# Performance work log

Measured on AMD Instinct MI355X. Metric: run time of the kernel, lower is better.

## Reference

```python
import jax, jax.numpy as jnp
import numpy as np

TOP_K = 2
EPS = 1e-9


def setup_inputs() -> dict:
    key = jax.random.key(0)
    k1, k2, k3, k4 = jax.random.split(key, 4)
    B, T, D, H, E = 4, 2048, 1024, 4096, 8
    x = jax.random.normal(k1, (B, T, D), dtype=jnp.float32)
    Wr = jax.random.normal(k2, (D, E), dtype=jnp.float32) * 0.02
    W1 = jax.random.normal(k3, (E, D, H), dtype=jnp.float32) * 0.02
    W2 = jax.random.normal(k4, (E, H, D), dtype=jnp.float32) * 0.02
    return {"x": x, "Wr": Wr, "W1": W1, "W2": W2}


def reference(x, Wr, W1, W2):
    # x: (B,T,D); Wr: (D,E); W1: (E,D,H); W2: (E,H,D)
    E = Wr.shape[1]
    logits = jnp.einsum('btd,de->bte', x, Wr)          # (B,T,E)
    probs = jax.nn.softmax(logits, axis=-1)
    top_p, top_i = jax.lax.top_k(probs, TOP_K)         # (B,T,K)
    gates = top_p / (jnp.sum(top_p, axis=-1, keepdims=True) + EPS)
    # combine weights per expert: (B,T,E), zero where expert not selected
    oh = jax.nn.one_hot(top_i, E, dtype=x.dtype)       # (B,T,K,E)
    comb = jnp.sum(oh * gates[..., None], axis=2)      # (B,T,E)
    out = jnp.zeros_like(x)
    for e in range(E):  # fixed small expert loop
        h = jax.nn.gelu(jnp.einsum('btd,dh->bth', x, W1[e]), approximate=False)
        y = jnp.einsum('bth,hd->btd', h, W2[e])
        out = out + comb[..., e:e + 1] * y
    # load-balancing loss (on detached stats, matching torch .detach())
    mask = (jnp.sum(oh, axis=2) > 0).astype(jnp.float32)  # (B,T,E)
    imp = jnp.sum(jax.lax.stop_gradient(probs), axis=(0, 1))
    load = jnp.sum(jax.lax.stop_gradient(mask), axis=(0, 1))
    imp = imp / (jnp.sum(imp) + EPS)
    load = load / (jnp.sum(load) + EPS)
    lb = jnp.sum(imp * load) * E
    return out, lb
```

## Files before the change

### kernel.cpp

```cpp
#include <hip/hip_runtime.h>
#include <hip/hip_bf16.h>
#include <math.h>

#define NTOK 8192
#define DDIM 1024
#define HDIM 4096
#define NEXP 8
#define HROWS (NTOK*2 + 256)
#define RBLK 512

typedef unsigned int u32;
typedef unsigned short u16;
typedef __bf16 bf16x8 __attribute__((ext_vector_type(8)));
typedef float f32x4 __attribute__((ext_vector_type(4)));
typedef u32 u32x4 __attribute__((ext_vector_type(4)));
typedef u16 u16x8 __attribute__((ext_vector_type(8)));
typedef u16 u16x4 __attribute__((ext_vector_type(4)));

__device__ __forceinline__ u16 f2bf(float f){
  u32 u = __builtin_bit_cast(u32, f);
  u32 r = (u + 0x7FFFu + ((u >> 16) & 1u)) >> 16;
  return (u16)r;
}
__device__ __forceinline__ float bf2f(u16 b){
  u32 u = ((u32)b) << 16;
  return __builtin_bit_cast(float, u);
}
__device__ __forceinline__ void gl_lds16(const void* g, void* l){
  __builtin_amdgcn_global_load_lds(
      (const __attribute__((address_space(1))) u32*)g,
      (__attribute__((address_space(3))) u32*)l, 16, 0, 0);
}
__device__ __forceinline__ float gelu_t(float v){
  float u = v * (0.7978845608f + 0.0356774081f * v * v);
  float e = __expf(2.0f * u);
  float t = 1.0f - 2.0f / (e + 1.0f);
  return 0.5f * v * (1.0f + t);
}

__global__ __launch_bounds__(256) void transpose_cvt(const float* __restrict__ in,
                                                     u16* __restrict__ out,
                                                     int R, int C){
  int e = blockIdx.z;
  const float* pin = in + (long)e * R * C;
  u16* pout = out + (long)e * R * C;
  __shared__ u16 tile[64][65];
  int c0 = blockIdx.x * 64, r0 = blockIdx.y * 64;
  int tid = threadIdx.x;
#pragma unroll
  for (int j = 0; j < 4; j++){
    int idx = tid + 256 * j;
    int r = idx >> 4, c4 = (idx & 15) << 2;
    float4 v = *(const float4*)(pin + (long)(r0 + r) * C + c0 + c4);
    tile[r][c4]     = f2bf(v.x);
    tile[r][c4 + 1] = f2bf(v.y);
    tile[r][c4 + 2] = f2bf(v.z);
    tile[r][c4 + 3] = f2bf(v.w);
  }
  __syncthreads();
#pragma unroll
  for (int j = 0; j < 4; j++){
    int idx = tid + 256 * j;
    int orow = idx >> 4, c4 = (idx & 15) << 2;
    u16x4 o;
    o[0] = tile[c4][orow];     o[1] = tile[c4 + 1][orow];
    o[2] = tile[c4 + 2][orow]; o[3] = tile[c4 + 3][orow];
    *(u16x4*)(pout + (long)(c0 + orow) * R + r0 + c4) = o;
  }
}

__global__ __launch_bounds__(1024) void route_kernel(const float* __restrict__ x,
                                                     const float* __restrict__ Wr,
                                                     u16* __restrict__ xb,
                                                     int4* __restrict__ meta,
                                                     float2* __restrict__ gates,
                                                     int* __restrict__ selrk,
                                                     int* __restrict__ blockhist,
                                                     float* __restrict__ impPart){
  const int wid = threadIdx.x >> 6;
  const int lane = threadIdx.x & 63;
  const int t = blockIdx.x * 16 + wid;
  const float* xr = x + (long)t * DDIM;
  u16* xbr = xb + (long)t * DDIM;
  float acc[NEXP] = {};
  for (int d0 = lane * 4; d0 < DDIM; d0 += 256){
    float4 xv = *(const float4*)(xr + d0);
    u16x4 xo;
    xo[0] = f2bf(xv.x); xo[1] = f2bf(xv.y); xo[2] = f2bf(xv.z); xo[3] = f2bf(xv.w);
    *(u16x4*)(xbr + d0) = xo;
    const float* w = Wr + d0 * NEXP;
#pragma unroll
    for (int q = 0; q < 4; q++){
      float xq = ((const float*)&xv)[q];
      float4 w0 = *(const float4*)(w + q * NEXP);
      float4 w1 = *(const float4*)(w + q * NEXP + 4);
      acc[0] += xq * w0.x; acc[1] += xq * w0.y; acc[2] += xq * w0.z; acc[3] += xq * w0.w;
      acc[4] += xq * w1.x; acc[5] += xq * w1.y; acc[6] += xq * w1.z; acc[7] += xq * w1.w;
    }
  }
#pragma unroll
  for (int e = 0; e < NEXP; e++){
#pragma unroll
    for (int off = 32; off; off >>= 1) acc[e] += __shfl_xor(acc[e], off, 64);
  }
  __shared__ int sel_s[32];
  __shared__ float p_s[16][NEXP];
  if (lane == 0){
    float mx = acc[0];
#pragma unroll
    for (int e = 1; e < NEXP; e++) mx = fmaxf(mx, acc[e]);
    float p[NEXP]; float s = 0.f;
#pragma unroll
    for (int e = 0; e < NEXP; e++){ p[e] = expf(acc[e] - mx); s += p[e]; }
    float inv = 1.f / s;
#pragma unroll
    for (int e = 0; e < NEXP; e++){ p[e] *= inv; p_s[wid][e] = p[e]; }
    int i0 = 0; float v0 = p[0];
#pragma unroll
    for (int e = 1; e < NEXP; e++) if (p[e] > v0){ v0 = p[e]; i0 = e; }
    int i1 = -1; float v1 = -1.f;
#pragma unroll
    for (int e = 0; e < NEXP; e++) if (e != i0 && p[e] > v1){ v1 = p[e]; i1 = e; }
    float gs = v0 + v1 + 1e-9f;
    meta[t] = make_int4(i0, i1, 0, 0);
    gates[t] = make_float2(v0 / gs, v1 / gs);
    sel_s[wid * 2] = i0;
    sel_s[wid * 2 + 1] = i1;
  }
  __syncthreads();
  const int tid = threadIdx.x;
  if (tid < 32){
    int e = sel_s[tid];
    int r = 0;
    for (int m = 0; m < tid; m++) r += (sel_s[m] == e) ? 1 : 0;
    selrk[blockIdx.x * 32 + tid] = (r << 3) | e;
  }
  if (tid < NEXP){
    int hcount = 0;
#pragma unroll
    for (int m = 0; m < 32; m++) hcount += (sel_s[m] == tid) ? 1 : 0;
    blockhist[blockIdx.x * NEXP + tid] = hcount;
    float s = 0.f;
#pragma unroll
    for (int w = 0; w < 16; w++) s += p_s[w][tid];
    impPart[blockIdx.x * NEXP + tid] = s;
  }
}

__global__ __launch_bounds__(512) void scan_kernel(int* __restrict__ blockhist,
                                                   const float* __restrict__ impPart,
                                                   int* __restrict__ cnt,
                                                   int* __restrict__ offs,
                                                   float* __restrict__ imp){
  const int e = threadIdx.x >> 6;
  const int lane = threadIdx.x & 63;
  const int base = lane * 8;
  int v[8]; int s = 0;
#pragma unroll
  for (int i = 0; i < 8; i++){
    int tmp = blockhist[(base + i) * NEXP + e];
    v[i] = s; s += tmp;
  }
  int inc = s;
#pragma unroll
  for (int off = 1; off < 64; off <<= 1){
    int o = __shfl_up(inc, off, 64);
    if (lane >= off) inc += o;
  }
  int excl = inc - s;
#pragma unroll
  for (int i = 0; i < 8; i++) blockhist[(base + i) * NEXP + e] = v[i] + excl;
  int tot = __shfl(inc, 63, 64);
  float fs = 0.f;
#pragma unroll
  for (int i = 0; i < 8; i++) fs += impPart[(base + i) * NEXP + e];
#pragma unroll
  for (int off = 32; off; off >>= 1) fs += __shfl_xor(fs, off, 64);
  __shared__ int cnt_s[NEXP];
  if (lane == 0){ cnt_s[e] = tot; cnt[e] = tot; imp[e] = fs; }
  __syncthreads();
  if (threadIdx.x == 0){
    int o = 0;
    for (int q = 0; q < NEXP; q++){ offs[q] = o; o += cnt_s[q]; }
  }
}

__global__ __launch_bounds__(256) void fill_kernel(const int* __restrict__ selrk,
                                                   const int* __restrict__ blockhist,
                                                   int* __restrict__ elist,
                                                   int4* __restrict__ meta){
  int m = blockIdx.x * 256 + threadIdx.x;
  int t = m >> 1, c = m & 1, b = m >> 5;
  int pk = selrk[m];
  int e = pk & 7, r = pk >> 3;
  int gslot = blockhist[b * NEXP + e] + r;
  elist[e * NTOK + gslot] = t;
  ((int*)meta)[t * 4 + 2 + c] = gslot;
}

template<int KD, int ND, int TG, bool GATHER, bool GELU>
__global__ __launch_bounds__(512, 4) void gemm_tb(const u16* __restrict__ Ag,
                                                  const u16* __restrict__ Bg,
                                                  u16* __restrict__ Cg,
                                                  const int* __restrict__ elist,
                                                  const int* __restrict__ cnt,
                                                  const int* __restrict__ offs){
  const int NDB = ND / 256;
  const int bid = blockIdx.x;
  const int e  = bid & 7;
  const int le = bid >> 3;
  const int tti = le % TG;
  const int db  = (le / TG) % NDB;
  const int tg  = le / (TG * NDB);
  const int tt  = tg * TG + tti;
  const int n_e = cnt[e];
  if (tt * 128 >= n_e) return;
  const int cb = db * 256;
  __shared__ __align__(16) u16 As[3][128 * 32];
  __shared__ __align__(16) u16 Bs[3][256 * 32];
  const int tid = threadIdx.x;
  const int sch = (((tid & 3) ^ ((tid >> 2) & 3) ^ ((tid >> 4) & 3)) << 3);
  const int row0 = offs[e] + tt * 128;
  long agb;
  {
    int row = tid >> 2;
    int arow;
    if (GATHER){
      int slot = tt * 128 + row;
      if (slot >= n_e) slot = n_e - 1;
      arow = elist[e * NTOK + slot];
    } else {
      arow = row0 + row;
    }
    agb = (long)arow * KD + sch;
  }
  const long bbase = ((long)e * ND + cb) * KD;
  const long bgb0 = bbase + (long)(tid >> 2) * KD + sch;
  const long bgb1 = bbase + (long)(128 + (tid >> 2)) * KD + sch;
  const int ldst = tid * 8;

  const int l = tid & 63;
  const int w = tid >> 6;
  const int wm = w >> 2, wn = w & 3;
  const int fr = l & 15, fq = l >> 4;
  const int swz = ((fq ^ (fr & 3) ^ ((fr >> 2) & 3)) << 4);
  const u32 aB0 = (u32)(uintptr_t)&As[0][0] + (u32)((wm * 64 + fr) * 64 + swz);
  const u32 bB0 = (u32)(uintptr_t)&Bs[0][0] + (u32)((wn * 64 + fr) * 64 + swz);

  f32x4 acc[4][4] = {};
  const int NK = KD / 32;

#define STG(cbuf, kel) \
    gl_lds16(Ag + agb + (kel), &As[cbuf][ldst]); \
    gl_lds16(Bg + bgb0 + (kel), &Bs[cbuf][ldst]); \
    gl_lds16(Bg + bgb1 + (kel), &Bs[cbuf][4096 + ldst]);

  STG(0, 0)
  STG(1, 32)
  asm volatile("s_waitcnt vmcnt(3)" ::: "memory");
  __builtin_amdgcn_s_barrier();

  int c = 0;
  for (int k = 0; k < NK; ++k){
    if (k + 2 < NK){
      int cn = c + 2; if (cn >= 3) cn -= 3;
      STG(cn, (k + 2) * 32)
    }
    const u32 aA = aB0 + (u32)(c * 8192);
    const u32 bA = bB0 + (u32)(c * 16384);
    u32x4 a[4], b[4];
    asm volatile("ds_read_b128 %0, %1"             : "=v"(a[0]) : "v"(aA));
    asm volatile("ds_read_b128 %0, %1 offset:1024" : "=v"(a[1]) : "v"(aA));
    asm volatile("ds_read_b128 %0, %1 offset:2048" : "=v"(a[2]) : "v"(aA));
    asm volatile("ds_read_b128 %0, %1 offset:3072" : "=v"(a[3]) : "v"(aA));
    asm volatile("ds_read_b128 %0, %1"             : "=v"(b[0]) : "v"(bA));
    asm volatile("ds_read_b128 %0, %1 offset:1024" : "=v"(b[1]) : "v"(bA));
    asm volatile("ds_read_b128 %0, %1 offset:2048" : "=v"(b[2]) : "v"(bA));
    asm volatile("ds_read_b128 %0, %1 offset:3072" : "=v"(b[3]) : "v"(bA));
    asm volatile("s_waitcnt lgkmcnt(0)" ::: "memory");
    __builtin_amdgcn_sched_barrier(0);
#pragma unroll
    for (int m = 0; m < 4; m++)
#pragma unroll
      for (int n = 0; n < 4; n++)
        acc[m][n] = __builtin_amdgcn_mfma_f32_16x16x32_bf16(
            __builtin_bit_cast(bf16x8, a[m]), __builtin_bit_cast(bf16x8, b[n]),
            acc[m][n], 0, 0, 0);
    if (k + 2 < NK){
      asm volatile("s_waitcnt vmcnt(3)" ::: "memory");
    } else if (k + 1 < NK){
      asm volatile("s_waitcnt vmcnt(0)" ::: "memory");
    }
    if (k + 1 < NK) __builtin_amdgcn_s_barrier();
    c += 1; if (c >= 3) c -= 3;
  }
#undef STG

#pragma unroll
  for (int m = 0; m < 4; m++){
#pragma unroll
    for (int j = 0; j < 4; j++){
      int row = wm * 64 + m * 16 + fq * 4 + j;
      int slot = tt * 128 + row;
      if (slot >= n_e) continue;
      long base = (long)(row0 + row) * ND + cb + wn * 64;
#pragma unroll
      for (int n = 0; n < 4; n++){
        float v = acc[m][n][j];
        if (GELU) v = gelu_t(v);
        Cg[base + n * 16 + fr] = f2bf(v);
      }
    }
  }
}

__global__ __launch_bounds__(256) void combine_kernel(const u16* __restrict__ ypair,
                                                      const int4* __restrict__ meta,
                                                      const float2* __restrict__ gates,
                                                      const int* __restrict__ offs,
                                                      float* __restrict__ out){
  int t = blockIdx.x;
  int c = threadIdx.x;
  int4 m = meta[t];
  float2 g = gates[t];
  long p0 = (long)(offs[m.x] + m.z) * DDIM + c * 4;
  long p1 = (long)(offs[m.y] + m.w) * DDIM + c * 4;
  u16x4 y0 = *(const u16x4*)&ypair[p0];
  u16x4 y1 = *(const u16x4*)&ypair[p1];
  float4 o;
  o.x = g.x * bf2f(y0[0]) + g.y * bf2f(y1[0]);
  o.y = g.x * bf2f(y0[1]) + g.y * bf2f(y1[1]);
  o.z = g.x * bf2f(y0[2]) + g.y * bf2f(y1[2]);
  o.w = g.x * bf2f(y0[3]) + g.y * bf2f(y1[3]);
  *(float4*)&out[(long)t * DDIM + c * 4] = o;
}

__global__ void lb_kernel(const float* __restrict__ imp, const int* __restrict__ cnt,
                          float* __restrict__ outp){
  if (threadIdx.x == 0 && blockIdx.x == 0){
    float si = 0.f, sl = 0.f;
    for (int e = 0; e < NEXP; e++){ si += imp[e]; sl += (float)cnt[e]; }
    float lb = 0.f;
    for (int e = 0; e < NEXP; e++)
      lb += (imp[e] / (si + 1e-9f)) * ((float)cnt[e] / (sl + 1e-9f));
    outp[0] = lb * (float)NEXP;
  }
}

extern "C" void kernel_launch(void* const* d_in, const int* in_sizes, int n_in,
                              void* d_out, int out_size, void* d_ws, size_t ws_size,
                              hipStream_t stream){
  const float* x  = (const float*)d_in[0];
  const float* Wr = (const float*)d_in[1];
  const float* W1 = (const float*)d_in[2];
  const float* W2 = (const float*)d_in[3];
  float* out = (float*)d_out;
  char* ws = (char*)d_ws;
  size_t off = 0;
  u16* xb = (u16*)(ws + off);   off += (size_t)NTOK * DDIM * 2;
  u16* wt = (u16*)(ws + off);   off += (size_t)NEXP * DDIM * HDIM * 2;
  u16* h  = (u16*)(ws + off);   off += (size_t)HROWS * HDIM * 2;
  u16* yp = (u16*)(ws + off);   off += (size_t)NTOK * 2 * DDIM * 2;
  int* elist    = (int*)(ws + off);    off += (size_t)NEXP * NTOK * 4;
  int4* meta    = (int4*)(ws + off);   off += (size_t)NTOK * 16;
  float2* gts   = (float2*)(ws + off); off += (size_t)NTOK * 8;
  int* selrk    = (int*)(ws + off);    off += (size_t)NTOK * 2 * 4;
  int* bhist    = (int*)(ws + off);    off += (size_t)RBLK * NEXP * 4;
  float* impP   = (float*)(ws + off);  off += (size_t)RBLK * NEXP * 4;
  int* cnt      = (int*)(ws + off);    off += 32;
  float* imp    = (float*)(ws + off);  off += 32;
  int* offs     = (int*)(ws + off);    off += 32;
  if (ws_size < off) return;

  route_kernel<<<RBLK, 1024, 0, stream>>>(x, Wr, xb, meta, gts, selrk, bhist, impP);
  scan_kernel<<<1, 512, 0, stream>>>(bhist, impP, cnt, offs, imp);
  fill_kernel<<<NTOK * 2 / 256, 256, 0, stream>>>(selrk, bhist, elist, meta);
  transpose_cvt<<<dim3(HDIM / 64, DDIM / 64, NEXP), 256, 0, stream>>>(W1, wt, DDIM, HDIM);
  gemm_tb<DDIM, HDIM, 8, true, true><<<NEXP * 64 * (HDIM / 256), 512, 0, stream>>>(
      xb, wt, h, elist, cnt, offs);
  transpose_cvt<<<dim3(DDIM / 64, HDIM / 64, NEXP), 256, 0, stream>>>(W2, wt, HDIM, DDIM);
  gemm_tb<HDIM, DDIM, 2, false, false><<<NEXP * 64 * (DDIM / 256), 512, 0, stream>>>(
      h, wt, yp, elist, cnt, offs);
  combine_kernel<<<NTOK, 256, 0, stream>>>(yp, meta, gts, offs, out);
  lb_kernel<<<1, 64, 0, stream>>>(imp, cnt, out + (size_t)NTOK * DDIM);
}
```

Baseline: 517.2 us.

## Enlarge GEMM tile to 256x256 and interleave LDS reads with MFMAs

The expert GEMM tile grows from 128x256 to 256x256 rows, so each wave now computes a 128x64 block with twice the accumulators. This doubles reuse of each loaded B tile and cuts global traffic per flop. The global prefetch is moved after the LDS reads, and graded lgkmcnt waits let the MFMAs for each row start as soon as that fragment arrives. In exchange, register and LDS use per block rise (occupancy hint drops from 4 to 2), there are fewer blocks, and more padding is wasted on each expert's last tile.

```diff
diff --git a/kernel.cpp b/kernel.cpp
--- a/kernel.cpp
+++ b/kernel.cpp
@@ -199,44 +199,46 @@
 }
 
 template<int KD, int ND, int TG, bool GATHER, bool GELU>
-__global__ __launch_bounds__(512, 4) void gemm_tb(const u16* __restrict__ Ag,
+__global__ __launch_bounds__(512, 2) void gemm_tb(const u16* __restrict__ Ag,
                                                   const u16* __restrict__ Bg,
                                                   u16* __restrict__ Cg,
                                                   const int* __restrict__ elist,
                                                   const int* __restrict__ cnt,
                                                   const int* __restrict__ offs){
-  const int NDB = ND / 256;
+  const int NBT = ND / 256;
   const int bid = blockIdx.x;
   const int e  = bid & 7;
   const int le = bid >> 3;
   const int tti = le % TG;
-  const int db  = (le / TG) % NDB;
-  const int tg  = le / (TG * NDB);
+  const int nb  = (le / TG) % NBT;
+  const int tg  = le / (TG * NBT);
   const int tt  = tg * TG + tti;
   const int n_e = cnt[e];
-  if (tt * 128 >= n_e) return;
-  const int cb = db * 256;
-  __shared__ __align__(16) u16 As[3][128 * 32];
+  if (tt * 256 >= n_e) return;
+  const int cb = nb * 256;
+  __shared__ __align__(16) u16 As[3][256 * 32];
   __shared__ __align__(16) u16 Bs[3][256 * 32];
   const int tid = threadIdx.x;
   const int sch = (((tid & 3) ^ ((tid >> 2) & 3) ^ ((tid >> 4) & 3)) << 3);
-  const int row0 = offs[e] + tt * 128;
-  long agb;
-  {
-    int row = tid >> 2;
+  const int row0 = offs[e] + tt * 256;
+  long agb[2];
+#pragma unroll
+  for (int i = 0; i < 2; i++){
+    int row = i * 128 + (tid >> 2);
     int arow;
     if (GATHER){
-      int slot = tt * 128 + row;
+      int slot = tt * 256 + row;
       if (slot >= n_e) slot = n_e - 1;
       arow = elist[e * NTOK + slot];
     } else {
       arow = row0 + row;
     }
-    agb = (long)arow * KD + sch;
-  }
-  const long bbase = ((long)e * ND + cb) * KD;
-  const long bgb0 = bbase + (long)(tid >> 2) * KD + sch;
-  const long bgb1 = bbase + (long)(128 + (tid >> 2)) * KD + sch;
+    agb[i] = (long)arow * KD + sch;
+  }
+  long bgb[2];
+#pragma unroll
+  for (int j = 0; j < 2; j++)
+    bgb[j] = ((long)e * ND + cb + j * 128 + (tid >> 2)) * KD + sch;
   const int ldst = tid * 8;
 
   const int l = tid & 63;
@@ -244,50 +246,65 @@
   const int wm = w >> 2, wn = w & 3;
   const int fr = l & 15, fq = l >> 4;
   const int swz = ((fq ^ (fr & 3) ^ ((fr >> 2) & 3)) << 4);
-  const u32 aB0 = (u32)(uintptr_t)&As[0][0] + (u32)((wm * 64 + fr) * 64 + swz);
+  const u32 aB0 = (u32)(uintptr_t)&As[0][0] + (u32)((wm * 128 + fr) * 64 + swz);
   const u32 bB0 = (u32)(uintptr_t)&Bs[0][0] + (u32)((wn * 64 + fr) * 64 + swz);
 
-  f32x4 acc[4][4] = {};
+  f32x4 acc[8][4] = {};
   const int NK = KD / 32;
 
 #define STG(cbuf, kel) \
-    gl_lds16(Ag + agb + (kel), &As[cbuf][ldst]); \
-    gl_lds16(Bg + bgb0 + (kel), &Bs[cbuf][ldst]); \
-    gl_lds16(Bg + bgb1 + (kel), &Bs[cbuf][4096 + ldst]);
+    gl_lds16(Ag + agb[0] + (kel), &As[cbuf][ldst]); \
+    gl_lds16(Ag + agb[1] + (kel), &As[cbuf][4096 + ldst]); \
+    gl_lds16(Bg + bgb[0] + (kel), &Bs[cbuf][ldst]); \
+    gl_lds16(Bg + bgb[1] + (kel), &Bs[cbuf][4096 + ldst]);
 
   STG(0, 0)
   STG(1, 32)
-  asm volatile("s_waitcnt vmcnt(3)" ::: "memory");
+  asm volatile("s_waitcnt vmcnt(4)" ::: "memory");
   __builtin_amdgcn_s_barrier();
 
   int c = 0;
   for (int k = 0; k < NK; ++k){
-    if (k + 2 < NK){
-      int cn = c + 2; if (cn >= 3) cn -= 3;
-      STG(cn, (k + 2) * 32)
-    }
-    const u32 aA = aB0 + (u32)(c * 8192);
+    const u32 aA = aB0 + (u32)(c * 16384);
     const u32 bA = bB0 + (u32)(c * 16384);
-    u32x4 a[4], b[4];
+    u32x4 a[8], b[4];
+    asm volatile("ds_read_b128 %0, %1"             : "=v"(b[0]) : "v"(bA));
+    asm volatile("ds_read_b128 %0, %1 offset:1024" : "=v"(b[1]) : "v"(bA));
+    asm volatile("ds_read_b128 %0, %1 offset:2048" : "=v"(b[2]) : "v"(bA));
+    asm volatile("ds_read_b128 %0, %1 offset:3072" : "=v"(b[3]) : "v"(bA));
     asm volatile("ds_read_b128 %0, %1"             : "=v"(a[0]) : "v"(aA));
     asm volatile("ds_read_b128 %0, %1 offset:1024" : "=v"(a[1]) : "v"(aA));
     asm volatile("ds_read_b128 %0, %1 offset:2048" : "=v"(a[2]) : "v"(aA));
     asm volatile("ds_read_b128 %0, %1 offset:3072" : "=v"(a[3]) : "v"(aA));
-    asm volatile("ds_read_b128 %0, %1"             : "=v"(b[0]) : "v"(bA));
-    asm volatile("ds_read_b128 %0, %1 offset:1024" : "=v"(b[1]) : "v"(bA));
-    asm volatile("ds_read_b128 %0, %1 offset:2048" : "=v"(b[2]) : "v"(bA));
-    asm volatile("ds_read_b128 %0, %1 offset:3072" : "=v"(b[3]) : "v"(bA));
-    asm volatile("s_waitcnt lgkmcnt(0)" ::: "memory");
-    __builtin_amdgcn_sched_barrier(0);
-#pragma unroll
-    for (int m = 0; m < 4; m++)
+    asm volatile("ds_read_b128 %0, %1 offset:4096" : "=v"(a[4]) : "v"(aA));
+    asm volatile("ds_read_b128 %0, %1 offset:5120" : "=v"(a[5]) : "v"(aA));
+    asm volatile("ds_read_b128 %0, %1 offset:6144" : "=v"(a[6]) : "v"(aA));
+    asm volatile("ds_read_b128 %0, %1 offset:7168" : "=v"(a[7]) : "v"(aA));
+    if (k + 2 < NK){
+      int cn = c + 2; if (cn >= 3) cn -= 3;
+      STG(cn, (k + 2) * 32)
+    }
+#pragma unroll
+    for (int m = 0; m < 8; m++){
+      switch (7 - m){
+        case 7: asm volatile("s_waitcnt lgkmcnt(7)" ::: "memory"); break;
+        case 6: asm volatile("s_waitcnt lgkmcnt(6)" ::: "memory"); break;
+        case 5: asm volatile("s_waitcnt lgkmcnt(5)" ::: "memory"); break;
+        case 4: asm volatile("s_waitcnt lgkmcnt(4)" ::: "memory"); break;
+        case 3: asm volatile("s_waitcnt lgkmcnt(3)" ::: "memory"); break;
+        case 2: asm volatile("s_waitcnt lgkmcnt(2)" ::: "memory"); break;
+        case 1: asm volatile("s_waitcnt lgkmcnt(1)" ::: "memory"); break;
+        case 0: asm volatile("s_waitcnt lgkmcnt(0)" ::: "memory"); break;
+      }
+      __builtin_amdgcn_sched_barrier(0);
 #pragma unroll
       for (int n = 0; n < 4; n++)
         acc[m][n] = __builtin_amdgcn_mfma_f32_16x16x32_bf16(
             __builtin_bit_cast(bf16x8, a[m]), __builtin_bit_cast(bf16x8, b[n]),
             acc[m][n], 0, 0, 0);
+    }
     if (k + 2 < NK){
-      asm volatile("s_waitcnt vmcnt(3)" ::: "memory");
+      asm volatile("s_waitcnt vmcnt(4)" ::: "memory");
     } else if (k + 1 < NK){
       asm volatile("s_waitcnt vmcnt(0)" ::: "memory");
     }
@@ -297,11 +314,11 @@
 #undef STG
 
 #pragma unroll
-  for (int m = 0; m < 4; m++){
+  for (int m = 0; m < 8; m++){
 #pragma unroll
     for (int j = 0; j < 4; j++){
-      int row = wm * 64 + m * 16 + fq * 4 + j;
-      int slot = tt * 128 + row;
+      int row = wm * 128 + m * 16 + fq * 4 + j;
+      int slot = tt * 256 + row;
       if (slot >= n_e) continue;
       long base = (long)(row0 + row) * ND + cb + wn * 64;
 #pragma unroll
@@ -376,10 +393,10 @@
   scan_kernel<<<1, 512, 0, stream>>>(bhist, impP, cnt, offs, imp);
   fill_kernel<<<NTOK * 2 / 256, 256, 0, stream>>>(selrk, bhist, elist, meta);
   transpose_cvt<<<dim3(HDIM / 64, DDIM / 64, NEXP), 256, 0, stream>>>(W1, wt, DDIM, HDIM);
-  gemm_tb<DDIM, HDIM, 8, true, true><<<NEXP * 64 * (HDIM / 256), 512, 0, stream>>>(
+  gemm_tb<DDIM, HDIM, 8, true, true><<<NEXP * (NTOK / 256) * (HDIM / 256), 512, 0, stream>>>(
       xb, wt, h, elist, cnt, offs);
   transpose_cvt<<<dim3(DDIM / 64, HDIM / 64, NEXP), 256, 0, stream>>>(W2, wt, HDIM, DDIM);
-  gemm_tb<HDIM, DDIM, 2, false, false><<<NEXP * 64 * (DDIM / 256), 512, 0, stream>>>(
+  gemm_tb<HDIM, DDIM, 2, false, false><<<NEXP * (NTOK / 256) * (DDIM / 256), 512, 0, stream>>>(
       h, wt, yp, elist, cnt, offs);
   combine_kernel<<<NTOK, 256, 0, stream>>>(yp, meta, gts, offs, out);
   lb_kernel<<<1, 64, 0, stream>>>(imp, cnt, out + (size_t)NTOK * DDIM);
```

New measurement: 581.9 us. 12.5% more time.
